# Performance work log

Measured on AMD Instinct MI355X. Metric: run time of the kernel, lower is better.

## Reference

```python
import jax, jax.numpy as jnp
import numpy as np

HIDDEN = 1024
N_HEADS = 16
HEAD_DIM = HIDDEN // N_HEADS


def apply_rope(x, freqs):
    # x: [b, s, h, d]; freqs: [s, d//2]
    b, s, h, d = x.shape
    x2 = x.reshape(b, s, h, d // 2, 2)
    x_real, x_imag = x2[..., 0], x2[..., 1]
    cos = jnp.cos(freqs)[None, :, None, :]  # [1, s, 1, d//2]
    sin = jnp.sin(freqs)[None, :, None, :]
    out_real = x_real * cos - x_imag * sin
    out_imag = x_real * sin + x_imag * cos
    return jnp.stack([out_real, out_imag], axis=-1).reshape(b, s, h, d)


def setup_inputs() -> dict:
    key = jax.random.key(0)
    k_x, k_f, k_wq, k_bq, k_wo, k_bo = jax.random.split(key, 6)
    b, s = 2, 2048
    x = jax.random.normal(k_x, (b, s, HIDDEN), dtype=jnp.float32)
    freqs = jax.random.normal(k_f, (s, HEAD_DIM // 2), dtype=jnp.float32)
    lim = 1.0 / np.sqrt(HIDDEN)
    W_qkv = jax.random.uniform(k_wq, (HIDDEN, 3 * HIDDEN), jnp.float32, -lim, lim)
    b_qkv = jax.random.uniform(k_bq, (3 * HIDDEN,), jnp.float32, -lim, lim)
    W_out = jax.random.uniform(k_wo, (HIDDEN, HIDDEN), jnp.float32, -lim, lim)
    b_out = jax.random.uniform(k_bo, (HIDDEN,), jnp.float32, -lim, lim)
    return {"x": x, "freqs": freqs, "W_qkv": W_qkv, "b_qkv": b_qkv,
            "W_out": W_out, "b_out": b_out}


def reference(x, freqs, W_qkv, b_qkv, W_out, b_out):
    b, s, c = x.shape
    h, d = N_HEADS, HEAD_DIM
    qkv = jnp.einsum('bsc,cf->bsf', x, W_qkv) + b_qkv  # [b, s, 3*c]
    qkv = qkv.reshape(b, s, 3, h, d)
    q, k, v = qkv[:, :, 0], qkv[:, :, 1], qkv[:, :, 2]  # [b, s, h, d]
    q = apply_rope(q, freqs)
    k = apply_rope(k, freqs)
    scale = 1.0 / np.sqrt(d).astype(np.float32)
    scores = jnp.einsum('bqhd,bkhd->bhqk', q, k) * scale  # [b, h, s, s]
    attn = jax.nn.softmax(scores, axis=-1)
    out = jnp.einsum('bhqk,bkhd->bqhd', attn, v).reshape(b, s, c)
    return jnp.einsum('bsc,cf->bsf', out, W_out) + b_out
```

## Files before the change

### kernel.cpp

```cpp
#include <hip/hip_runtime.h>
#include <math.h>

constexpr int kB = 2;
constexpr int kS = 2048;
constexpr int kC = 1024;
constexpr int kH = 16;
constexpr int kD = 64;
constexpr int kF = 3072;
constexpr int kT = kB * kS;

typedef __attribute__((ext_vector_type(8))) short short8v;
typedef __attribute__((ext_vector_type(4))) short short4v;
typedef __attribute__((ext_vector_type(4))) float f32x4;
typedef __attribute__((ext_vector_type(16))) float f32x16;

__device__ __forceinline__ short f2bf(float f) {
    unsigned u = __builtin_bit_cast(unsigned, f);
    u += 0x7fffu + ((u >> 16) & 1u);
    return (short)(u >> 16);
}

__device__ __forceinline__ unsigned cvtpk(float a, float b) {
    unsigned r;
    asm("v_cvt_pk_bf16_f32 %0, %1, %2" : "=v"(r) : "v"(a), "v"(b));
    return r;
}

__device__ __forceinline__ unsigned pk_bf16(float a, float b) {
    unsigned ua = __builtin_bit_cast(unsigned, a);
    ua += 0x7fffu + ((ua >> 16) & 1u);
    unsigned ub = __builtin_bit_cast(unsigned, b);
    ub += 0x7fffu + ((ub >> 16) & 1u);
    return (ua >> 16) | (ub & 0xffff0000u);
}

__device__ __forceinline__ void gl_lds16(const void* g, void* l) {
    __builtin_amdgcn_global_load_lds(
        (const __attribute__((address_space(1))) char*)g,
        (__attribute__((address_space(3))) char*)l, 16, 0, 0);
}

__device__ __forceinline__ f32x4 mfma16(short8v a, short8v b, f32x4 c) {
    return __builtin_amdgcn_mfma_f32_16x16x32_bf16(a, b, c, 0, 0, 0);
}
__device__ __forceinline__ f32x16 mfma32(short8v a, short8v b, f32x16 c) {
    return __builtin_amdgcn_mfma_f32_32x32x16_bf16(a, b, c, 0, 0, 0);
}

__global__ __launch_bounds__(256) void cvt_x_kernel(const float* __restrict__ in,
                                                    short* __restrict__ out, int n4) {
    int i = blockIdx.x * 256 + threadIdx.x;
    if (i < n4) {
        float4 v = reinterpret_cast<const float4*>(in)[i];
        short4v o = { f2bf(v.x), f2bf(v.y), f2bf(v.z), f2bf(v.w) };
        reinterpret_cast<short4v*>(out)[i] = o;
    }
}

__global__ __launch_bounds__(256) void tcvt_kernel(const float* __restrict__ w,
                                                   short* __restrict__ wt, int K, int N) {
    __shared__ float Ts[64][65];
    const int t = threadIdx.x;
    const int n0 = blockIdx.x * 64, k0 = blockIdx.y * 64;
    const int r = t >> 4, c4 = (t & 15) * 4;
#pragma unroll
    for (int rr = 0; rr < 64; rr += 16) {
        float4 v = *reinterpret_cast<const float4*>(&w[(size_t)(k0 + r + rr) * N + n0 + c4]);
        Ts[r + rr][c4 + 0] = v.x; Ts[r + rr][c4 + 1] = v.y;
        Ts[r + rr][c4 + 2] = v.z; Ts[r + rr][c4 + 3] = v.w;
    }
    __syncthreads();
#pragma unroll
    for (int rr = 0; rr < 64; rr += 16) {
        int n = r + rr;
        short4v o = { f2bf(Ts[c4 + 0][n]), f2bf(Ts[c4 + 1][n]),
                      f2bf(Ts[c4 + 2][n]), f2bf(Ts[c4 + 3][n]) };
        *reinterpret_cast<short4v*>(&wt[(size_t)(n0 + n) * K + k0 + c4]) = o;
    }
}

__global__ __launch_bounds__(256) void rope_tab_kernel(const float* __restrict__ freqs,
                                                       float* __restrict__ cost,
                                                       float* __restrict__ sint) {
    int i = blockIdx.x * 256 + threadIdx.x;
    float f = freqs[i];
    float s, c;
    sincosf(f, &s, &c);
    cost[i] = c; sint[i] = s;
}

__device__ __forceinline__ void gemm_main(const short* __restrict__ A,
                                          const short* __restrict__ Bt,
                                          int m0, int n0, short* Als, short* Bls,
                                          f32x4 acc[4][4]) {
    const int tid = threadIdx.x, wid = tid >> 6, lane = tid & 63;
    const int srow = lane >> 3, schunk = lane & 7;
    const int fr = lane & 15, fg = lane >> 4;
    const int wm = (wid >> 1) * 64, wn = (wid & 1) * 64;
    for (int kt = 0; kt < 1024; kt += 64) {
        __syncthreads();
#pragma unroll
        for (int j = 0; j < 4; ++j) {
            int i = wid * 4 + j;
            int row = i * 8 + srow;
            gl_lds16(&A[(size_t)(m0 + row) * 1024 + kt + ((schunk ^ (row & 7)) << 3)],
                     &Als[i * 512]);
        }
#pragma unroll
        for (int j = 0; j < 4; ++j) {
            int i = wid * 4 + j;
            int row = i * 8 + srow;
            gl_lds16(&Bt[(size_t)(n0 + row) * 1024 + kt + ((schunk ^ (row & 7)) << 3)],
                     &Bls[i * 512]);
        }
        __syncthreads();
#pragma unroll
        for (int kk = 0; kk < 2; ++kk) {
            short8v af[4], bf[4];
#pragma unroll
            for (int fm = 0; fm < 4; ++fm) {
                int row = wm + fm * 16 + fr;
                af[fm] = *reinterpret_cast<const short8v*>(
                    &Als[row * 64 + (((fg + 4 * kk) ^ (row & 7)) << 3)]);
            }
#pragma unroll
            for (int fn = 0; fn < 4; ++fn) {
                int row = wn + fn * 16 + fr;
                bf[fn] = *reinterpret_cast<const short8v*>(
                    &Bls[row * 64 + (((fg + 4 * kk) ^ (row & 7)) << 3)]);
            }
#pragma unroll
            for (int fm = 0; fm < 4; ++fm)
#pragma unroll
                for (int fn = 0; fn < 4; ++fn)
                    acc[fm][fn] = mfma16(af[fm], bf[fn], acc[fm][fn]);
        }
    }
}

__global__ __launch_bounds__(256) void qkv_gemm_kernel(
    const short* __restrict__ xb, const short* __restrict__ wqt,
    const float* __restrict__ bias, const float* __restrict__ cost,
    const float* __restrict__ sint,
    short* __restrict__ qg, short* __restrict__ kg, short* __restrict__ vt) {
    __shared__ __attribute__((aligned(16))) short Als[128 * 64];
    __shared__ __attribute__((aligned(16))) short Bls[128 * 64];
    f32x4 acc[4][4] = {};
    const int tid = threadIdx.x, wid = tid >> 6, lane = tid & 63;
    const int m0 = blockIdx.y * 128, n0 = blockIdx.x * 128;
    gemm_main(xb, wqt, m0, n0, Als, Bls, acc);

    const int fr = lane & 15, fg = lane >> 4;
    const int wm = (wid >> 1) * 64, wn = (wid & 1) * 64;
    const int which = (n0 + wn) >> 10;
    const int bidx = m0 >> 11;
#pragma unroll
    for (int fn = 0; fn < 4; ++fn) {
        int col = n0 + wn + fn * 16 + fr;
        float bv = bias[col];
        int d = col & 63;
        int h = (col >> 6) & 15;
        int p0 = d >> 1;
        int odd = d & 1;
#pragma unroll
        for (int fm = 0; fm < 4; ++fm) {
            int r0 = m0 + wm + fm * 16 + fg * 4;
            int s0 = r0 & 2047;
            float c[4];
#pragma unroll
            for (int r = 0; r < 4; ++r) c[r] = acc[fm][fn][r] + bv;
            if (which < 2) {
#pragma unroll
                for (int r = 0; r < 4; ++r) {
                    float cs = cost[(s0 + r) * 32 + p0];
                    float sn = sint[(s0 + r) * 32 + p0];
                    float p = __shfl_xor(c[r], 1);
                    float o = odd ? fmaf(p, sn, c[r] * cs) : fmaf(-p, sn, c[r] * cs);
                    c[r] = (which == 0) ? o * 0.1803368801f : o;
                }
                short* dst = which ? kg : qg;
                size_t base = ((size_t)(bidx * 16 + h) * 2048 + s0) * 64 + d;
#pragma unroll
                for (int r = 0; r < 4; ++r) dst[base + (size_t)r * 64] = f2bf(c[r]);
            } else {
                short4v o = { f2bf(c[0]), f2bf(c[1]), f2bf(c[2]), f2bf(c[3]) };
                *reinterpret_cast<short4v*>(
                    &vt[((size_t)(bidx * 16 + h) * 64 + d) * 2048 + s0]) = o;
            }
        }
    }
}

__global__ __launch_bounds__(256, 4) void attn_mfma_kernel(
    const short* __restrict__ qg, const short* __restrict__ kg,
    const short* __restrict__ vt, short* __restrict__ ab) {
    __shared__ __attribute__((aligned(16))) short LDSBUF[16384];
    const int tid = threadIdx.x, wid = tid >> 6, lane = tid & 63;
    const int l31 = lane & 31, hi = lane >> 5;
    const int p = wid >> 1;
    const int wq = wid & 1;
    const int r8 = lane >> 3, c8 = lane & 7;
    const int soff = 8 * (c8 ^ r8);

    const int bid = blockIdx.x;
    const int swz = (bid & 7) * 128 + (bid >> 3);
    const int bh = swz >> 5;
    const int q0 = (swz & 31) * 64 + wq * 32;

    const short* qb = qg + (size_t)bh * 2048 * 64;
    const short* kb = kg + (size_t)bh * 2048 * 64;
    const short* vb = vt + (size_t)bh * 64 * 2048;

    short8v qf[4];
#pragma unroll
    for (int kkq = 0; kkq < 4; ++kkq)
        qf[kkq] = *reinterpret_cast<const short8v*>(
            &qb[(size_t)(q0 + l31) * 64 + kkq * 16 + hi * 8]);

    f32x16 o[2] = {};
    float l_i = 0.f;

    auto stage = [&](int t, int buf) {
        const int kt = t * 32;
        short* Kd = LDSBUF + buf * 8192 + p * 2048 + (wq * 8) * 64;
        const short* Ks = kb + (size_t)(p * 1024 + kt) * 64;
#pragma unroll
        for (int j = 0; j < 2; ++j) {
            int row = j * 16 + wq * 8 + r8;
            gl_lds16(Ks + (size_t)row * 64 + soff, Kd + j * 1024);
        }
        short* Vd = LDSBUF + buf * 8192 + 4096 + (wid * 8) * 64;
        const int s = c8 ^ r8;
#pragma unroll
        for (int j = 0; j < 2; ++j) {
            int d = j * 32 + wid * 8 + r8;
            gl_lds16(vb + (size_t)d * 2048 + (s >> 2) * 1024 + kt + (s & 3) * 8,
                     Vd + j * 2048);
        }
    };

    stage(0, 0);
    __syncthreads();

    for (int t = 0; t < 32; ++t) {
        const int buf = t & 1;
        if (t + 1 < 32) stage(t + 1, buf ^ 1);
        const short* Kb = LDSBUF + buf * 8192 + p * 2048;
        const short* Vb = LDSBUF + buf * 8192 + 4096;

        f32x16 sacc = {};
#pragma unroll
        for (int kkq = 0; kkq < 4; ++kkq) {
            short8v a = *reinterpret_cast<const short8v*>(
                &Kb[l31 * 64 + (((kkq * 2 + hi) ^ (l31 & 7)) << 3)]);
            sacc = mfma32(a, qf[kkq], sacc);
        }

#pragma unroll
        for (int r = 0; r < 16; ++r) sacc[r] = __builtin_amdgcn_exp2f(sacc[r]);
        float t8[8];
#pragma unroll
        for (int r = 0; r < 8; ++r) t8[r] = sacc[r] + sacc[r + 8];
        float t4[4];
#pragma unroll
        for (int r = 0; r < 4; ++r) t4[r] = t8[r] + t8[r + 4];
        float rs = (t4[0] + t4[1]) + (t4[2] + t4[3]);
        rs += __shfl_xor(rs, 32);
        l_i += rs;

        unsigned c[8];
#pragma unroll
        for (int i = 0; i < 8; ++i) c[i] = cvtpk(sacc[2 * i], sacc[2 * i + 1]);
        short8v pb[2];
#pragma unroll
        for (int kk = 0; kk < 2; ++kk) {
            unsigned a0 = c[kk * 4 + 0], a1 = c[kk * 4 + 1];
            unsigned a2 = c[kk * 4 + 2], a3 = c[kk * 4 + 3];
            unsigned s0x = (unsigned)__shfl_xor((int)a0, 32);
            unsigned s1x = (unsigned)__shfl_xor((int)a1, 32);
            unsigned s2x = (unsigned)__shfl_xor((int)a2, 32);
            unsigned s3x = (unsigned)__shfl_xor((int)a3, 32);
            uint4 w;
            w.x = hi ? s2x : a0;
            w.y = hi ? s3x : a1;
            w.z = hi ? a2 : s0x;
            w.w = hi ? a3 : s1x;
            pb[kk] = __builtin_bit_cast(short8v, w);
        }

#pragma unroll
        for (int kk = 0; kk < 2; ++kk) {
            short8v v0 = *reinterpret_cast<const short8v*>(
                &Vb[l31 * 64 + (((p * 4 + kk * 2 + hi) ^ (l31 & 7)) << 3)]);
            short8v v1 = *reinterpret_cast<const short8v*>(
                &Vb[(32 + l31) * 64 + (((p * 4 + kk * 2 + hi) ^ (l31 & 7)) << 3)]);
            o[0] = mfma32(v0, pb[kk], o[0]);
            o[1] = mfma32(v1, pb[kk], o[1]);
        }
        __syncthreads();
    }

    float* olds = reinterpret_cast<float*>(LDSBUF + 4096);
    float* lls  = olds + 2 * 2304;
    if (p == 1) {
        float* ob = olds + wq * 2304 + lane * 36;
#pragma unroll
        for (int i = 0; i < 4; ++i) {
            f32x4 w0 = { o[0][4 * i + 0], o[0][4 * i + 1], o[0][4 * i + 2], o[0][4 * i + 3] };
            *reinterpret_cast<f32x4*>(ob + i * 4) = w0;
            f32x4 w1 = { o[1][4 * i + 0], o[1][4 * i + 1], o[1][4 * i + 2], o[1][4 * i + 3] };
            *reinterpret_cast<f32x4*>(ob + 16 + i * 4) = w1;
        }
        lls[wq * 64 + lane] = l_i;
    }
    __syncthreads();
    if (p == 0) {
        float* ob = olds + wq * 2304 + lane * 36;
#pragma unroll
        for (int i = 0; i < 4; ++i) {
            f32x4 w0 = *reinterpret_cast<const f32x4*>(ob + i * 4);
            f32x4 w1 = *reinterpret_cast<const f32x4*>(ob + 16 + i * 4);
#pragma unroll
            for (int j = 0; j < 4; ++j) {
                o[0][4 * i + j] += w0[j];
                o[1][4 * i + j] += w1[j];
            }
        }
        l_i += lls[wq * 64 + lane];

        const float inv = 1.f / l_i;
        short* ep = LDSBUF + wid * 2048;
        const int q = l31;
#pragma unroll
        for (int fd = 0; fd < 2; ++fd)
#pragma unroll
            for (int i = 0; i < 4; ++i) {
                int d0 = fd * 32 + 8 * i + 4 * hi;
                uint2 w;
                w.x = pk_bf16(o[fd][4 * i + 0] * inv, o[fd][4 * i + 1] * inv);
                w.y = pk_bf16(o[fd][4 * i + 2] * inv, o[fd][4 * i + 3] * inv);
                *reinterpret_cast<uint2*>(&ep[q * 64 + (d0 ^ (8 * (q & 3)))]) = w;
            }
        __builtin_amdgcn_s_waitcnt(0);
        const int bb = bh >> 4, hh = bh & 15;
        const int wrow = r8, wcol = c8;
#pragma unroll
        for (int j = 0; j < 4; ++j) {
            int row = j * 8 + wrow;
            short8v tv = *reinterpret_cast<const short8v*>(
                &ep[row * 64 + ((8 * wcol) ^ (8 * (row & 3)))]);
            int s = q0 + row;
            *reinterpret_cast<short8v*>(
                &ab[(size_t)(bb * 2048 + s) * 1024 + hh * 64 + 8 * wcol]) = tv;
        }
    }
}

__global__ __launch_bounds__(256) void out_gemm_kernel(
    const short* __restrict__ ab, const short* __restrict__ wot,
    const float* __restrict__ bias, float* __restrict__ out) {
    __shared__ __attribute__((aligned(16))) short Als[128 * 64];
    __shared__ __attribute__((aligned(16))) short Bls[128 * 64];
    f32x4 acc[4][4] = {};
    const int tid = threadIdx.x, wid = tid >> 6, lane = tid & 63;
    const int m0 = blockIdx.y * 128, n0 = blockIdx.x * 128;
    gemm_main(ab, wot, m0, n0, Als, Bls, acc);
    const int fr = lane & 15, fg = lane >> 4;
    const int wm = (wid >> 1) * 64, wn = (wid & 1) * 64;
#pragma unroll
    for (int fn = 0; fn < 4; ++fn) {
        int col = n0 + wn + fn * 16 + fr;
        float bv = bias[col];
#pragma unroll
        for (int fm = 0; fm < 4; ++fm) {
            int r0 = m0 + wm + fm * 16 + fg * 4;
#pragma unroll
            for (int r = 0; r < 4; ++r)
                out[(size_t)(r0 + r) * 1024 + col] = acc[fm][fn][r] + bv;
        }
    }
}

extern "C" void kernel_launch(void* const* d_in, const int* in_sizes, int n_in,
                              void* d_out, int out_size, void* d_ws, size_t ws_size,
                              hipStream_t stream) {
    const float* x     = (const float*)d_in[0];
    const float* freqs = (const float*)d_in[1];
    const float* W_qkv = (const float*)d_in[2];
    const float* b_qkv = (const float*)d_in[3];
    const float* W_out = (const float*)d_in[4];
    const float* b_out = (const float*)d_in[5];
    float* out = (float*)d_out;

    char* w = (char*)d_ws;
    short* xb  = (short*)w;  w += (size_t)kT * kC * 2;
    short* wqt = (short*)w;  w += (size_t)kF * kC * 2;
    short* wot = (short*)w;  w += (size_t)kC * kC * 2;
    short* qgw = (short*)w;  w += (size_t)kB * kH * kS * kD * 2;
    short* kgw = (short*)w;  w += (size_t)kB * kH * kS * kD * 2;
    short* vtw = (short*)w;  w += (size_t)kB * kH * kS * kD * 2;
    short* abw = (short*)w;  w += (size_t)kT * kC * 2;
    float* costt = (float*)w; w += (size_t)kS * (kD / 2) * 4;
    float* sintt = (float*)w; w += (size_t)kS * (kD / 2) * 4;

    cvt_x_kernel<<<dim3(kT * kC / 1024), 256, 0, stream>>>(x, xb, kT * kC / 4);
    tcvt_kernel<<<dim3(kF / 64, kC / 64), 256, 0, stream>>>(W_qkv, wqt, kC, kF);
    tcvt_kernel<<<dim3(kC / 64, kC / 64), 256, 0, stream>>>(W_out, wot, kC, kC);
    rope_tab_kernel<<<dim3(kS * (kD / 2) / 256), 256, 0, stream>>>(freqs, costt, sintt);

    qkv_gemm_kernel<<<dim3(kF / 128, kT / 128), 256, 0, stream>>>(
        xb, wqt, b_qkv, costt, sintt, qgw, kgw, vtw);
    attn_mfma_kernel<<<dim3(1024), 256, 0, stream>>>(qgw, kgw, vtw, abw);
    out_gemm_kernel<<<dim3(kC / 128, kT / 128), 256, 0, stream>>>(abw, wot, b_out, out);
}
```

Baseline: 139.6 us.

## Merge prep kernels into one launch and software-pipeline the attention loop

Folds the four preprocessing launches (x conversion, two weight transpose-converts, rope table) into a single kernel that dispatches on block index, removing launch gaps. In the attention kernel, the loop is skewed by one iteration: the PV MFMAs for tile t-1 run alongside the QK MFMAs for tile t, and fragments are read into registers before the barrier so the next stage can refill the freed buffer. This aims to overlap the exp/convert/shuffle work with matrix ops. In exchange it holds more live registers (pb_prev, K/V fragments), which could lower occupancy, and the prep kernel's uniform shared-memory allocation applies to every block.

```diff
diff --git a/kernel.cpp b/kernel.cpp
--- a/kernel.cpp
+++ b/kernel.cpp
@@ -47,21 +47,10 @@
     return __builtin_amdgcn_mfma_f32_32x32x16_bf16(a, b, c, 0, 0, 0);
 }
 
-__global__ __launch_bounds__(256) void cvt_x_kernel(const float* __restrict__ in,
-                                                    short* __restrict__ out, int n4) {
-    int i = blockIdx.x * 256 + threadIdx.x;
-    if (i < n4) {
-        float4 v = reinterpret_cast<const float4*>(in)[i];
-        short4v o = { f2bf(v.x), f2bf(v.y), f2bf(v.z), f2bf(v.w) };
-        reinterpret_cast<short4v*>(out)[i] = o;
-    }
-}
-
-__global__ __launch_bounds__(256) void tcvt_kernel(const float* __restrict__ w,
-                                                   short* __restrict__ wt, int K, int N) {
-    __shared__ float Ts[64][65];
-    const int t = threadIdx.x;
-    const int n0 = blockIdx.x * 64, k0 = blockIdx.y * 64;
+__device__ __forceinline__ void tcvt_body(const float* __restrict__ w,
+                                          short* __restrict__ wt, int K, int N,
+                                          int bx, int by, int t, float Ts[64][65]) {
+    const int n0 = bx * 64, k0 = by * 64;
     const int r = t >> 4, c4 = (t & 15) * 4;
 #pragma unroll
     for (int rr = 0; rr < 64; rr += 16) {
@@ -79,14 +68,32 @@
     }
 }
 
-__global__ __launch_bounds__(256) void rope_tab_kernel(const float* __restrict__ freqs,
-                                                       float* __restrict__ cost,
-                                                       float* __restrict__ sint) {
-    int i = blockIdx.x * 256 + threadIdx.x;
-    float f = freqs[i];
-    float s, c;
-    sincosf(f, &s, &c);
-    cost[i] = c; sint[i] = s;
+__global__ __launch_bounds__(256) void prep_kernel(
+    const float* __restrict__ x, short* __restrict__ xb,
+    const float* __restrict__ wq, short* __restrict__ wqt,
+    const float* __restrict__ wo, short* __restrict__ wot,
+    const float* __restrict__ freqs, float* __restrict__ cost,
+    float* __restrict__ sint) {
+    __shared__ float Ts[64][65];
+    const int bid = blockIdx.x, t = threadIdx.x;
+    if (bid < 4096) {
+        int i = bid * 256 + t;
+        float4 v = reinterpret_cast<const float4*>(x)[i];
+        short4v o = { f2bf(v.x), f2bf(v.y), f2bf(v.z), f2bf(v.w) };
+        reinterpret_cast<short4v*>(xb)[i] = o;
+    } else if (bid < 4864) {
+        int i = bid - 4096;
+        tcvt_body(wq, wqt, kC, kF, i % 48, i / 48, t, Ts);
+    } else if (bid < 5120) {
+        int i = bid - 4864;
+        tcvt_body(wo, wot, kC, kC, i % 16, i / 16, t, Ts);
+    } else {
+        int i = (bid - 5120) * 256 + t;
+        float f = freqs[i];
+        float s, c;
+        sincosf(f, &s, &c);
+        cost[i] = c; sint[i] = s;
+    }
 }
 
 __device__ __forceinline__ void gemm_main(const short* __restrict__ A,
@@ -242,60 +249,73 @@
     stage(0, 0);
     __syncthreads();
 
-    for (int t = 0; t < 32; ++t) {
-        const int buf = t & 1;
-        if (t + 1 < 32) stage(t + 1, buf ^ 1);
-        const short* Kb = LDSBUF + buf * 8192 + p * 2048;
-        const short* Vb = LDSBUF + buf * 8192 + 4096;
+    short8v pb_prev[2];
+    for (int t = 0; t <= 32; ++t) {
+        const int cur = t & 1, prv = cur ^ 1;
+        short8v kf[4], vf0[2], vf1[2];
+        if (t < 32) {
+            const short* Kb = LDSBUF + cur * 8192 + p * 2048;
+#pragma unroll
+            for (int kkq = 0; kkq < 4; ++kkq)
+                kf[kkq] = *reinterpret_cast<const short8v*>(
+                    &Kb[l31 * 64 + (((kkq * 2 + hi) ^ (l31 & 7)) << 3)]);
+        }
+        if (t > 0) {
+            const short* Vb = LDSBUF + prv * 8192 + 4096;
+#pragma unroll
+            for (int kk = 0; kk < 2; ++kk) {
+                vf0[kk] = *reinterpret_cast<const short8v*>(
+                    &Vb[l31 * 64 + (((p * 4 + kk * 2 + hi) ^ (l31 & 7)) << 3)]);
+                vf1[kk] = *reinterpret_cast<const short8v*>(
+                    &Vb[(32 + l31) * 64 + (((p * 4 + kk * 2 + hi) ^ (l31 & 7)) << 3)]);
+            }
+        }
+        __syncthreads();
+        if (t + 1 < 32) stage(t + 1, prv);
 
         f32x16 sacc = {};
-#pragma unroll
-        for (int kkq = 0; kkq < 4; ++kkq) {
-            short8v a = *reinterpret_cast<const short8v*>(
-                &Kb[l31 * 64 + (((kkq * 2 + hi) ^ (l31 & 7)) << 3)]);
-            sacc = mfma32(a, qf[kkq], sacc);
-        }
-
-#pragma unroll
-        for (int r = 0; r < 16; ++r) sacc[r] = __builtin_amdgcn_exp2f(sacc[r]);
-        float t8[8];
-#pragma unroll
-        for (int r = 0; r < 8; ++r) t8[r] = sacc[r] + sacc[r + 8];
-        float t4[4];
-#pragma unroll
-        for (int r = 0; r < 4; ++r) t4[r] = t8[r] + t8[r + 4];
-        float rs = (t4[0] + t4[1]) + (t4[2] + t4[3]);
-        rs += __shfl_xor(rs, 32);
-        l_i += rs;
-
-        unsigned c[8];
-#pragma unroll
-        for (int i = 0; i < 8; ++i) c[i] = cvtpk(sacc[2 * i], sacc[2 * i + 1]);
-        short8v pb[2];
-#pragma unroll
-        for (int kk = 0; kk < 2; ++kk) {
-            unsigned a0 = c[kk * 4 + 0], a1 = c[kk * 4 + 1];
-            unsigned a2 = c[kk * 4 + 2], a3 = c[kk * 4 + 3];
-            unsigned s0x = (unsigned)__shfl_xor((int)a0, 32);
-            unsigned s1x = (unsigned)__shfl_xor((int)a1, 32);
-            unsigned s2x = (unsigned)__shfl_xor((int)a2, 32);
-            unsigned s3x = (unsigned)__shfl_xor((int)a3, 32);
-            uint4 w;
-            w.x = hi ? s2x : a0;
-            w.y = hi ? s3x : a1;
-            w.z = hi ? a2 : s0x;
-            w.w = hi ? a3 : s1x;
-            pb[kk] = __builtin_bit_cast(short8v, w);
-        }
-
-#pragma unroll
-        for (int kk = 0; kk < 2; ++kk) {
-            short8v v0 = *reinterpret_cast<const short8v*>(
-                &Vb[l31 * 64 + (((p * 4 + kk * 2 + hi) ^ (l31 & 7)) << 3)]);
-            short8v v1 = *reinterpret_cast<const short8v*>(
-                &Vb[(32 + l31) * 64 + (((p * 4 + kk * 2 + hi) ^ (l31 & 7)) << 3)]);
-            o[0] = mfma32(v0, pb[kk], o[0]);
-            o[1] = mfma32(v1, pb[kk], o[1]);
+        if (t < 32) {
+#pragma unroll
+            for (int kkq = 0; kkq < 4; ++kkq)
+                sacc = mfma32(kf[kkq], qf[kkq], sacc);
+        }
+        if (t > 0) {
+#pragma unroll
+            for (int kk = 0; kk < 2; ++kk) {
+                o[0] = mfma32(vf0[kk], pb_prev[kk], o[0]);
+                o[1] = mfma32(vf1[kk], pb_prev[kk], o[1]);
+            }
+        }
+        if (t < 32) {
+#pragma unroll
+            for (int r = 0; r < 16; ++r) sacc[r] = __builtin_amdgcn_exp2f(sacc[r]);
+            unsigned c[8];
+#pragma unroll
+            for (int i = 0; i < 8; ++i) c[i] = cvtpk(sacc[2 * i], sacc[2 * i + 1]);
+#pragma unroll
+            for (int kk = 0; kk < 2; ++kk) {
+                unsigned a0 = c[kk * 4 + 0], a1 = c[kk * 4 + 1];
+                unsigned a2 = c[kk * 4 + 2], a3 = c[kk * 4 + 3];
+                unsigned s0x = (unsigned)__shfl_xor((int)a0, 32);
+                unsigned s1x = (unsigned)__shfl_xor((int)a1, 32);
+                unsigned s2x = (unsigned)__shfl_xor((int)a2, 32);
+                unsigned s3x = (unsigned)__shfl_xor((int)a3, 32);
+                uint4 w;
+                w.x = hi ? s2x : a0;
+                w.y = hi ? s3x : a1;
+                w.z = hi ? a2 : s0x;
+                w.w = hi ? a3 : s1x;
+                pb_prev[kk] = __builtin_bit_cast(short8v, w);
+            }
+            float t8[8];
+#pragma unroll
+            for (int r = 0; r < 8; ++r) t8[r] = sacc[r] + sacc[r + 8];
+            float t4[4];
+#pragma unroll
+            for (int r = 0; r < 4; ++r) t4[r] = t8[r] + t8[r + 4];
+            float rs = (t4[0] + t4[1]) + (t4[2] + t4[3]);
+            rs += __shfl_xor(rs, 32);
+            l_i += rs;
         }
         __syncthreads();
     }
@@ -403,11 +423,8 @@
     float* costt = (float*)w; w += (size_t)kS * (kD / 2) * 4;
     float* sintt = (float*)w; w += (size_t)kS * (kD / 2) * 4;
 
-    cvt_x_kernel<<<dim3(kT * kC / 1024), 256, 0, stream>>>(x, xb, kT * kC / 4);
-    tcvt_kernel<<<dim3(kF / 64, kC / 64), 256, 0, stream>>>(W_qkv, wqt, kC, kF);
-    tcvt_kernel<<<dim3(kC / 64, kC / 64), 256, 0, stream>>>(W_out, wot, kC, kC);
-    rope_tab_kernel<<<dim3(kS * (kD / 2) / 256), 256, 0, stream>>>(freqs, costt, sintt);
-
+    prep_kernel<<<dim3(5376), 256, 0, stream>>>(x, xb, W_qkv, wqt, W_out, wot,
+                                                freqs, costt, sintt);
     qkv_gemm_kernel<<<dim3(kF / 128, kT / 128), 256, 0, stream>>>(
         xb, wqt, b_qkv, costt, sintt, qgw, kgw, vtw);
     attn_mfma_kernel<<<dim3(1024), 256, 0, stream>>>(qgw, kgw, vtw, abw);
```

Result: faster. 133.3 us (-4.5%).
